# Kernel tuning notes

Hardware: AMD Instinct MI355X
Metric: run time of the kernel (lower is better)

The kernel has to match this reference:

```python
import jax, jax.numpy as jnp
import numpy as np

B, S, H = 1, 2048, 1024
NH, NKV, D = 8, 2, 128           # query heads, kv heads, head_dim
E, TOPK = 64, 6                   # experts per modality, top-k
IT, IV, IS = 512, 256, 1024       # text / vision expert inter, shared inter (=512*2)
THETA = 500000.0
SECTIONS = (22, 22, 20)           # h, w, t rotary freq split; sum = D//2
EPS = 1e-5


def rmsnorm(x, w):
    return x * w * jax.lax.rsqrt(jnp.mean(x * x, axis=-1, keepdims=True) + EPS)


def apply_mrope(x, positions):
    # x: [B,S,h,D]; positions: [3,B,S] (h, w, t position streams)
    inv_freq = 1.0 / (THETA ** (jnp.arange(0, D, 2, dtype=jnp.float32) / D))  # [D//2]
    axis_idx = np.repeat(np.arange(3), SECTIONS)              # which pos stream per freq band
    pos = jnp.transpose(positions[axis_idx], (1, 2, 0)).astype(jnp.float32)  # [B,S,D//2]
    freqs = pos * inv_freq
    cos = jnp.cos(freqs)[:, :, None, :]
    sin = jnp.sin(freqs)[:, :, None, :]
    x1, x2 = x[..., 0::2], x[..., 1::2]                       # interleaved (non-neox)
    o1 = x1 * cos - x2 * sin
    o2 = x1 * sin + x2 * cos
    return jnp.stack([o1, o2], axis=-1).reshape(x.shape)


def attention(x, positions, w_qkv, w_o):
    b, s, _ = x.shape
    qkv = x @ w_qkv
    q, k, v = jnp.split(qkv, [NH * D, NH * D + NKV * D], axis=-1)
    q = q.reshape(b, s, NH, D)
    k = k.reshape(b, s, NKV, D)
    v = v.reshape(b, s, NKV, D)
    q = apply_mrope(q, positions)
    k = apply_mrope(k, positions)
    rep = NH // NKV
    k = jnp.repeat(k, rep, axis=2)
    v = jnp.repeat(v, rep, axis=2)
    scores = jnp.einsum('bqhd,bkhd->bhqk', q, k) * (D ** -0.5)
    causal = jnp.tril(jnp.ones((s, s), bool))
    scores = jnp.where(causal, scores, -jnp.inf)
    attn = jax.nn.softmax(scores, axis=-1)
    out = jnp.einsum('bhqk,bkhd->bqhd', attn, v).reshape(b, s, NH * D)
    return out @ w_o


def mlp(x, wg, wu, wd):
    return (jax.nn.silu(x @ wg) * (x @ wu)) @ wd


def moe_branch(x, gate_w, bias, wg, wu, wd):
    # x: [T,H]; gate_w: [H,E] fp32; bias: [E] fp32 correction bias
    logits = x.astype(jnp.float32) @ gate_w                   # [T,E]
    scores = jax.nn.sigmoid(logits)
    _, topi = jax.lax.top_k(scores + bias[None, :], TOPK)     # bias only picks experts
    w = jnp.take_along_axis(scores, topi, axis=-1)            # weights from raw scores
    w = w / jnp.sum(w, axis=-1, keepdims=True)                # renormalize
    T = x.shape[0]
    gates = jnp.zeros((T, E), jnp.float32).at[jnp.arange(T)[:, None], topi].set(w)
    g = jax.nn.silu(jnp.einsum('th,ehi->eti', x, wg)) * jnp.einsum('th,ehi->eti', x, wu)
    g = g * gates.T[:, :, None].astype(x.dtype)               # fold routing weights pre-down-proj
    return jnp.einsum('eti,eih->th', g, wd)


def _forward(hidden_states, positions, visual_token_mask, w_qkv, w_o, ln1_w, ln2_w,
             text_gate_w, vision_gate_w, corr_bias, tw_gate, tw_up, tw_down,
             vw_gate, vw_up, vw_down, sw_gate, sw_up, sw_down):
    h = hidden_states + attention(rmsnorm(hidden_states, ln1_w), positions, w_qkv, w_o)
    x = rmsnorm(h, ln2_w).reshape(-1, H)                      # [T,H]
    shared = mlp(x, sw_gate, sw_up, sw_down)
    text_out = moe_branch(x, text_gate_w, corr_bias[0], tw_gate, tw_up, tw_down)
    vision_out = moe_branch(x, vision_gate_w, corr_bias[1], vw_gate, vw_up, vw_down)
    mask = visual_token_mask.reshape(-1, 1)
    moe_out = jnp.where(mask, vision_out, text_out) + shared
    return h + moe_out.reshape(h.shape)


def setup_inputs() -> dict:
    key = jax.random.key(0)
    ks = jax.random.split(key, 16)
    rn = lambda i, shape, s: jax.random.normal(ks[i], shape, jnp.float32) * s
    return dict(
        hidden_states=rn(0, (B, S, H), 1.0),
        positions=jnp.broadcast_to(jnp.arange(S, dtype=jnp.int32)[None, None, :], (3, B, S)),
        visual_token_mask=jax.random.bernoulli(ks[1], 0.3, (B, S)),
        w_qkv=rn(2, (H, (NH + 2 * NKV) * D), H ** -0.5),
        w_o=rn(3, (NH * D, H), (NH * D) ** -0.5),
        ln1_w=jnp.ones((H,), jnp.float32),
        ln2_w=jnp.ones((H,), jnp.float32),
        text_gate_w=rn(4, (H, E), H ** -0.5),
        vision_gate_w=rn(5, (H, E), H ** -0.5),
        corr_bias=rn(6, (2, E), 0.02),
        tw_gate=rn(7, (E, H, IT), H ** -0.5),
        tw_up=rn(8, (E, H, IT), H ** -0.5),
        tw_down=rn(9, (E, IT, H), IT ** -0.5),
        vw_gate=rn(10, (E, H, IV), H ** -0.5),
        vw_up=rn(11, (E, H, IV), H ** -0.5),
        vw_down=rn(12, (E, IV, H), IV ** -0.5),
        sw_gate=rn(13, (H, IS), H ** -0.5),
        sw_up=rn(14, (H, IS), H ** -0.5),
        sw_down=rn(15, (IS, H), IS ** -0.5),
    )


def reference(hidden_states, positions, visual_token_mask, w_qkv, w_o, ln1_w, ln2_w,
              text_gate_w, vision_gate_w, corr_bias, tw_gate, tw_up, tw_down,
              vw_gate, vw_up, vw_down, sw_gate, sw_up, sw_down):
    return _forward(hidden_states, positions, visual_token_mask, w_qkv, w_o, ln1_w, ln2_w,
                    text_gate_w, vision_gate_w, corr_bias, tw_gate, tw_up, tw_down,
                    vw_gate, vw_up, vw_down, sw_gate, sw_up, sw_down)
```

## Files before the change

kernel.cpp:

```cpp
#include <hip/hip_runtime.h>
#include <hip/hip_bf16.h>
#include <math.h>

#define TT   2048
#define HID  1024
#define NHEAD 8
#define NKVH  2
#define HD   128
#define QKVN 1536
#define NEXP 64
#define NTOP 6
#define I_T  512
#define I_V  256
#define I_S  1024
#define SBASE ((size_t)12288 * 512)
#define NCHUNK 576

typedef unsigned short u16;
typedef __attribute__((ext_vector_type(8))) short short8v;
typedef __attribute__((ext_vector_type(4))) float f32x4;

__device__ inline u16 f2bf(float f) {
  __hip_bfloat16 h = __float2bfloat16(f);
  return *reinterpret_cast<u16*>(&h);
}
__device__ inline float bfu2f(u16 u) {
  unsigned x = ((unsigned)u) << 16;
  return __uint_as_float(x);
}
__device__ inline void split2(float f, u16& h, u16& l) {
  h = f2bf(f);
  l = f2bf(f - bfu2f(h));
}
__device__ inline void split8(const float* f, u16* h, u16* l) {
#pragma unroll
  for (int i = 0; i < 8; ++i) split2(f[i], h[i], l[i]);
}

__device__ inline f32x4 mfma16(short8v a, short8v b, f32x4 c) {
  return __builtin_amdgcn_mfma_f32_16x16x32_bf16(a, b, c, 0, 0, 0);
}

__device__ inline void wload(const float* __restrict__ W, int ldw, int c0, int kc,
                             float4* r) {
  const int t = threadIdx.x;
  const int c4 = (t & 7) << 2;
  const int r0 = t >> 3;
#pragma unroll
  for (int j = 0; j < 4; ++j)
    r[j] = *(const float4*)&W[(size_t)(kc + r0 + j * 32) * ldw + c0 + c4];
}
__device__ inline void wwrite(const float4* r, u16* lds) {
  const int t = threadIdx.x;
  const int c4 = (t & 7) << 2;
  const int r0 = t >> 3;
#pragma unroll
  for (int j = 0; j < 4; ++j) {
    int k = r0 + j * 32;
    u16* dst = lds + ((k >> 3) * 32) * 8 + (k & 7);
    dst[(c4 + 0) * 8] = f2bf(r[j].x);
    dst[(c4 + 1) * 8] = f2bf(r[j].y);
    dst[(c4 + 2) * 8] = f2bf(r[j].z);
    dst[(c4 + 3) * 8] = f2bf(r[j].w);
  }
}

template<bool F32, bool BF, bool LO>
__global__ __launch_bounds__(256) void rmsnorm_kernel(const float* __restrict__ x,
                                                      const float* __restrict__ w,
                                                      float* __restrict__ o32,
                                                      u16* __restrict__ obfH,
                                                      u16* __restrict__ obfL) {
  const int row = blockIdx.x;
  const int t = threadIdx.x;
  const float4 v = *(const float4*)(x + (size_t)row * HID + t * 4);
  float ss = v.x*v.x + v.y*v.y + v.z*v.z + v.w*v.w;
#pragma unroll
  for (int m = 32; m >= 1; m >>= 1) ss += __shfl_xor(ss, m);
  __shared__ float red[4];
  __shared__ float rrs;
  if ((t & 63) == 0) red[t >> 6] = ss;
  __syncthreads();
  if (t == 0) rrs = rsqrtf((red[0] + red[1] + red[2] + red[3]) * (1.0f / HID) + 1e-5f);
  __syncthreads();
  const float rr = rrs;
  const float4 wv = *(const float4*)(w + t * 4);
  float o[4];
  o[0] = v.x * wv.x * rr; o[1] = v.y * wv.y * rr;
  o[2] = v.z * wv.z * rr; o[3] = v.w * wv.w * rr;
  if (F32) *(float4*)(o32 + (size_t)row * HID + t * 4) = *(float4*)o;
  if (BF) {
    u16 h[4], l[4];
#pragma unroll
    for (int i = 0; i < 4; ++i) split2(o[i], h[i], l[i]);
    *(uint2*)(obfH + (size_t)row * HID + t * 4) = *(uint2*)h;
    if (LO) *(uint2*)(obfL + (size_t)row * HID + t * 4) = *(uint2*)l;
  }
}

__global__ __launch_bounds__(256) void convert_w(const float* __restrict__ W, int N,
                                                 u16* __restrict__ PH,
                                                 u16* __restrict__ PL) {
  const int c = blockIdx.x * 256 + threadIdx.x;
  const int k8 = blockIdx.y;
  float f[8];
#pragma unroll
  for (int e = 0; e < 8; ++e) f[e] = W[(size_t)(k8 * 8 + e) * N + c];
  u16 h8[8], l8[8];
  split8(f, h8, l8);
  size_t gi = ((size_t)(c >> 5) * 128 + k8) * 256 + (size_t)(c & 31) * 8;
  *(uint4*)&PH[gi] = *(uint4*)h8;
  *(uint4*)&PL[gi] = *(uint4*)l8;
}

template<bool RES>
__global__ __launch_bounds__(256) void dense_split(const u16* __restrict__ AH,
                                                   const u16* __restrict__ AL,
                                                   const u16* __restrict__ WPH,
                                                   const u16* __restrict__ WPL,
                                                   const float* __restrict__ resid,
                                                   float* __restrict__ C, int N) {
  __shared__ u16 sWH[32768], sWL[32768];
  __shared__ u16 sAH[4096],  sAL[4096];
  const int t = threadIdx.x;
  const int cs = blockIdx.x;
  const int c0 = cs * 32;
  const int rows = TT / gridDim.y;
  const int mstart = blockIdx.y * rows, mend = mstart + rows;
  {
    const u16* gh = WPH + (size_t)cs * 32768;
    const u16* gl = WPL + (size_t)cs * 32768;
#pragma unroll
    for (int r = 0; r < 16; ++r) {
      int i8 = (t + 256 * r) * 8;
      *(uint4*)&sWH[i8] = *(const uint4*)&gh[i8];
      *(uint4*)&sWL[i8] = *(const uint4*)&gl[i8];
    }
  }
  const int w = t >> 6, lane = t & 63;
  const int rowHalf = (w & 1) << 4, colHalf = (w >> 1) << 4;
  for (int m0 = mstart; m0 < mend; m0 += 32) {
    f32x4 hh = {0.f,0.f,0.f,0.f}, hl = {0.f,0.f,0.f,0.f};
    f32x4 lh = {0.f,0.f,0.f,0.f}, ll = {0.f,0.f,0.f,0.f};
    for (int kc = 0; kc < HID; kc += 128) {
      __syncthreads();
#pragma unroll
      for (int r = 0; r < 2; ++r) {
        int task = t + 256 * r;
        int row = task >> 4, kg = task & 15;
        size_t g = (size_t)(m0 + row) * HID + kc + kg * 8;
        *(uint4*)&sAH[(kg * 32 + row) * 8] = *(const uint4*)&AH[g];
        *(uint4*)&sAL[(kg * 32 + row) * 8] = *(const uint4*)&AL[g];
      }
      __syncthreads();
#pragma unroll
      for (int ks = 0; ks < 4; ++ks) {
        int arow = rowHalf + (lane & 15);
        int akg = ks * 4 + (lane >> 4);
        short8v ah = *(const short8v*)&sAH[(akg * 32 + arow) * 8];
        short8v al = *(const short8v*)&sAL[(akg * 32 + arow) * 8];
        int wcol = colHalf + (lane & 15);
        int wkg = (kc >> 3) + ks * 4 + (lane >> 4);
        short8v bh = *(const short8v*)&sWH[(wkg * 32 + wcol) * 8];
        short8v bl = *(const short8v*)&sWL[(wkg * 32 + wcol) * 8];
        hh = mfma16(ah, bh, hh);
        hl = mfma16(ah, bl, hl);
        lh = mfma16(al, bh, lh);
        ll = mfma16(al, bl, ll);
      }
    }
    f32x4 acc = (hh + hl) + (lh + ll);
#pragma unroll
    for (int i = 0; i < 4; ++i) {
      int r = m0 + rowHalf + ((lane >> 4) << 2) + i;
      int c = c0 + colHalf + (lane & 15);
      float v = acc[i];
      if (RES) v += resid[(size_t)r * N + c];
      C[(size_t)r * N + c] = v;
    }
  }
}

__global__ __launch_bounds__(256) void pack_qkv(const float* __restrict__ qkv,
                                                const int* __restrict__ pos,
                                                u16* __restrict__ Qh, u16* __restrict__ Ql,
                                                u16* __restrict__ Kph, u16* __restrict__ Kpl,
                                                u16* __restrict__ Vph, u16* __restrict__ Vpl) {
  const int tile = blockIdx.x;
  const int t = threadIdx.x;
  __shared__ float cs[2048], sn[2048];
  for (int i = t; i < 2048; i += 256) {
    int tok32 = i >> 6, fi = i & 63;
    int tok = tile * 32 + tok32;
    int axis = (fi < 22) ? 0 : (fi < 44 ? 1 : 2);
    float posv = (float)pos[axis * TT + tok];
// ... 260 lines not shown
  float f[8];
#pragma unroll
  for (int j = 0; j < 8; ++j) f[j] = acc[j] * inv;
  split8(f, h8, l8);
  const size_t d = (size_t)(qb * 16 + row) * HID + head * HD + c8;
  *(uint4*)&aoH[d] = *(uint4*)h8;
  *(uint4*)&aoL[d] = *(uint4*)l8;
}

__global__ __launch_bounds__(256) void gate_kernel(const float* __restrict__ x2,
                                                   const int* __restrict__ vmask,
                                                   const float* __restrict__ tg,
                                                   const float* __restrict__ vg,
                                                   const float* __restrict__ cbias,
                                                   int* __restrict__ counts,
                                                   int* __restrict__ ptok,
                                                   float* __restrict__ pw) {
  const int tok = blockIdx.x;
  const int t = threadIdx.x;
  __shared__ float xs[HID];
  __shared__ float part[4][NEXP];
  __shared__ float sc[NEXP];
  __shared__ float sb[NEXP];
  *(float4*)&xs[t * 4] = *(const float4*)(x2 + (size_t)tok * HID + t * 4);
  __syncthreads();
  const int vis = (vmask[tok] != 0) ? 1 : 0;
  const float* gw = vis ? vg : tg;
  {
    const int e = t & 63, pr = t >> 6;
    float acc = 0.f;
    for (int h = pr * 256; h < (pr + 1) * 256; ++h) acc += xs[h] * gw[h * NEXP + e];
    part[pr][e] = acc;
  }
  __syncthreads();
  if (t < NEXP) {
    float a = part[0][t] + part[1][t] + part[2][t] + part[3][t];
    float s = 1.f / (1.f + expf(-a));
    sc[t] = s;
    sb[t] = s + cbias[vis * NEXP + t];
  }
  __syncthreads();
  if (t == 0) {
    int chosen[NTOP];
    unsigned long long usedm = 0ULL;
    float wsum = 0.f;
    for (int k = 0; k < NTOP; ++k) {
      float best = -1e30f; int bi = 0;
      for (int e = 0; e < NEXP; ++e) {
        if ((usedm >> e) & 1ULL) continue;
        if (sb[e] > best) { best = sb[e]; bi = e; }
      }
      usedm |= (1ULL << bi);
      chosen[k] = bi;
      wsum += sc[bi];
    }
    const float inv = 1.f / wsum;
    for (int k = 0; k < NTOP; ++k) {
      int e = chosen[k];
      int slot = vis * NEXP + e;
      int pos = atomicAdd(&counts[slot], 1);
      ptok[slot * TT + pos] = tok;
      pw[slot * TT + pos] = sc[e] * inv;
    }
  }
}

__global__ void scan_kernel(const int* __restrict__ counts, int* __restrict__ rowoff) {
  if (threadIdx.x == 0 && blockIdx.x == 0) {
    int s = 0;
    for (int i = 0; i < 128; ++i) { rowoff[i] = s; s += counts[i]; }
    rowoff[128] = s;
  }
}

template<int MODE>
__device__ inline void act_base(const int* rowoff, int slot, size_t& eb, int& stride) {
  if (MODE == 0) { eb = (size_t)rowoff[slot] * 512; stride = 512; }
  else if (MODE == 1) {
    int Rt = rowoff[64];
    eb = (size_t)Rt * 512 + (size_t)(rowoff[slot] - Rt) * 256; stride = 256;
  } else { eb = SBASE; stride = 1024; }
}

template<int IDIM, int MODE>
__global__ __launch_bounds__(256) void gateup_stream(const u16* __restrict__ X,
                                                     const float* __restrict__ WG,
                                                     const float* __restrict__ WU,
                                                     const int* __restrict__ counts,
                                                     const int* __restrict__ ptok,
                                                     const float* __restrict__ pw,
                                                     const int* __restrict__ rowoff,
                                                     u16* __restrict__ ACT) {
  __shared__ u16 sG[2][4096], sU[2][4096];
  __shared__ int toksL[256];
  __shared__ float twsL[256];
  const int c0 = blockIdx.x * 32;
  int cnt, mstart, mend, slot = 0;
  size_t eb; int stride;
  const float *wgp, *wup;
  if (MODE == 2) {
    cnt = TT; mstart = blockIdx.y * 256; mend = mstart + 256;
    eb = SBASE; stride = 1024;
    wgp = WG; wup = WU;
  } else {
    const int e = blockIdx.y;
    slot = (MODE == 1 ? NEXP : 0) + e;
    cnt = counts[slot];
    mstart = 0; mend = cnt;
    act_base<MODE>(rowoff, slot, eb, stride);
    wgp = WG + (size_t)e * HID * IDIM;
    wup = WU + (size_t)e * HID * IDIM;
  }
  if (mstart >= mend) return;
  const int w = threadIdx.x >> 6, lane = threadIdx.x & 63;
  const int lrow = lane & 15, loct = lane >> 4;

  for (int m0 = mstart; m0 < mend; m0 += 256) {
    {
      int gi = m0 + threadIdx.x;
      int tok = 0; float tw = 0.f;
      if (gi < cnt) {
        tok = (MODE == 2) ? gi : ptok[slot * TT + gi];
        tw  = (MODE == 2) ? 1.f : pw[slot * TT + gi];
      }
      toksL[threadIdx.x] = tok; twsL[threadIdx.x] = tw;
    }
    float4 rg[4], ru[4];
    wload(wgp, IDIM, c0, 0, rg);
    wload(wup, IDIM, c0, 0, ru);
    __syncthreads();
    wwrite(rg, sG[0]);
    wwrite(ru, sU[0]);
    const u16* xr[4];
#pragma unroll
    for (int tt = 0; tt < 4; ++tt)
      xr[tt] = X + (size_t)toksL[(w + tt * 4) * 16 + lrow] * HID;
    f32x4 aG[4][2], aU[4][2];
#pragma unroll
    for (int tt = 0; tt < 4; ++tt)
#pragma unroll
      for (int fr = 0; fr < 2; ++fr) {
        aG[tt][fr] = (f32x4){0.f,0.f,0.f,0.f};
        aU[tt][fr] = (f32x4){0.f,0.f,0.f,0.f};
      }
    __syncthreads();
    for (int c = 0; c < HID / 128; ++c) {
      const int cur = c & 1;
      if (c + 1 < HID / 128) {
        wload(wgp, IDIM, c0, (c + 1) * 128, rg);
        wload(wup, IDIM, c0, (c + 1) * 128, ru);
      }
#pragma unroll
      for (int ks = 0; ks < 4; ++ks) {
        const int boff = ((ks * 4 + loct) * 32 + lrow) * 8;
        short8v bg0 = *(const short8v*)&sG[cur][boff];
        short8v bg1 = *(const short8v*)&sG[cur][boff + 128];
        short8v bu0 = *(const short8v*)&sU[cur][boff];
        short8v bu1 = *(const short8v*)&sU[cur][boff + 128];
#pragma unroll
        for (int tt = 0; tt < 4; ++tt) {
          short8v a = *(const short8v*)&xr[tt][c * 128 + ks * 32 + loct * 8];
          aG[tt][0] = mfma16(a, bg0, aG[tt][0]);
          aG[tt][1] = mfma16(a, bg1, aG[tt][1]);
          aU[tt][0] = mfma16(a, bu0, aU[tt][0]);
          aU[tt][1] = mfma16(a, bu1, aU[tt][1]);
        }
      }
      if (c + 1 < HID / 128) {
        wwrite(rg, sG[cur ^ 1]);
        wwrite(ru, sU[cur ^ 1]);
      }
      __syncthreads();
    }
#pragma unroll
    for (int tt = 0; tt < 4; ++tt) {
      const int ti = w + tt * 4;
#pragma unroll
      for (int i = 0; i < 4; ++i) {
        const int r = loct * 4 + i;
        const int gi = m0 + ti * 16 + r;
        if (gi < cnt) {
          const float twv = twsL[ti * 16 + r];
#pragma unroll
          for (int fr = 0; fr < 2; ++fr) {
            float g = aG[tt][fr][i], u = aU[tt][fr][i];
            float a = g / (1.f + expf(-g)) * u * twv;
            ACT[eb + (size_t)gi * stride + c0 + fr * 16 + lrow] = f2bf(a);
          }
        }
      }
    }
    __syncthreads();
  }
}

template<int KDIM, int MODE>
__global__ __launch_bounds__(256) void down_stream(const u16* __restrict__ ACT,
                                                   const float* __restrict__ WD,
                                                   const int* __restrict__ counts,
                                                   const int* __restrict__ ptok,
                                                   const int* __restrict__ rowoff,
                                                   float* __restrict__ OUT) {
  __shared__ u16 sW[2][4096];
  __shared__ int toksL[256];
  const int c0 = blockIdx.x * 32;
  int cnt, mstart, mend, slot = 0;
  size_t eb; int stride;
  const float* wdp;
  if (MODE == 2) {
    cnt = TT; mstart = blockIdx.y * 256; mend = mstart + 256;
    eb = SBASE; stride = 1024;
    wdp = WD;
  } else {
    const int e = blockIdx.y;
    slot = (MODE == 1 ? NEXP : 0) + e;
    cnt = counts[slot];
    mstart = 0; mend = cnt;
    act_base<MODE>(rowoff, slot, eb, stride);
    wdp = WD + (size_t)e * KDIM * HID;
  }
  if (mstart >= mend) return;
  const int w = threadIdx.x >> 6, lane = threadIdx.x & 63;
  const int lrow = lane & 15, loct = lane >> 4;
  constexpr int NC = KDIM / 128;

  for (int m0 = mstart; m0 < mend; m0 += 256) {
    {
      int gi = m0 + threadIdx.x;
      int tok = 0;
      if (gi < cnt) tok = (MODE == 2) ? gi : ptok[slot * TT + gi];
      toksL[threadIdx.x] = tok;
    }
    float4 rw[4];
    wload(wdp, HID, c0, 0, rw);
    __syncthreads();
    wwrite(rw, sW[0]);
    const u16* ar[4];
#pragma unroll
    for (int tt = 0; tt < 4; ++tt) {
      int gi = m0 + (w + tt * 4) * 16 + lrow;
      int gc = (gi < cnt) ? gi : (cnt - 1);
      ar[tt] = ACT + eb + (size_t)gc * stride;
    }
    f32x4 acc[4][2];
#pragma unroll
    for (int tt = 0; tt < 4; ++tt)
#pragma unroll
      for (int fr = 0; fr < 2; ++fr) acc[tt][fr] = (f32x4){0.f,0.f,0.f,0.f};
    __syncthreads();
    for (int c = 0; c < NC; ++c) {
      const int cur = c & 1;
      if (c + 1 < NC) wload(wdp, HID, c0, (c + 1) * 128, rw);
#pragma unroll
      for (int ks = 0; ks < 4; ++ks) {
        const int boff = ((ks * 4 + loct) * 32 + lrow) * 8;
        short8v b0 = *(const short8v*)&sW[cur][boff];
        short8v b1 = *(const short8v*)&sW[cur][boff + 128];
#pragma unroll
        for (int tt = 0; tt < 4; ++tt) {
          short8v a = *(const short8v*)&ar[tt][c * 128 + ks * 32 + loct * 8];
          acc[tt][0] = mfma16(a, b0, acc[tt][0]);
          acc[tt][1] = mfma16(a, b1, acc[tt][1]);
        }
      }
      if (c + 1 < NC) wwrite(rw, sW[cur ^ 1]);
      __syncthreads();
    }
#pragma unroll
    for (int tt = 0; tt < 4; ++tt) {
      const int ti = w + tt * 4;
#pragma unroll
      for (int i = 0; i < 4; ++i) {
        const int r = loct * 4 + i;
        const int gi = m0 + ti * 16 + r;
        if (gi < cnt) {
          const int tok = toksL[ti * 16 + r];
#pragma unroll
          for (int fr = 0; fr < 2; ++fr)
            atomicAdd(&OUT[(size_t)tok * HID + c0 + fr * 16 + lrow], acc[tt][fr][i]);
        }
      }
    }
    __syncthreads();
  }
}

__global__ __launch_bounds__(256) void add2_kernel(const float* __restrict__ a,
                                                   const float* __restrict__ b,
                                                   float* __restrict__ out) {
  const size_t i = ((size_t)blockIdx.x * 256 + threadIdx.x) * 4;
  const float4 va = *(const float4*)(a + i);
  const float4 vb = *(const float4*)(b + i);
  float4 o;
  o.x = va.x + vb.x; o.y = va.y + vb.y; o.z = va.z + vb.z; o.w = va.w + vb.w;
  *(float4*)(out + i) = o;
}

extern "C" void kernel_launch(void* const* d_in, const int* in_sizes, int n_in,
                              void* d_out, int out_size, void* d_ws, size_t ws_size,
                              hipStream_t stream) {
  const float* hidden   = (const float*)d_in[0];
  const int*   positions= (const int*)d_in[1];
  const int*   vmask    = (const int*)d_in[2];
  const float* w_qkv    = (const float*)d_in[3];
  const float* w_o      = (const float*)d_in[4];
  const float* ln1      = (const float*)d_in[5];
  const float* ln2      = (const float*)d_in[6];
  const float* tgw      = (const float*)d_in[7];
  const float* vgw      = (const float*)d_in[8];
  const float* cbias    = (const float*)d_in[9];
  const float* twg      = (const float*)d_in[10];
  const float* twu      = (const float*)d_in[11];
  const float* twd      = (const float*)d_in[12];
  const float* vwg      = (const float*)d_in[13];
  const float* vwu      = (const float*)d_in[14];
  const float* vwd      = (const float*)d_in[15];
  const float* swg      = (const float*)d_in[16];
  const float* swu      = (const float*)d_in[17];
  const float* swd      = (const float*)d_in[18];
  float* out = (float*)d_out;

  char* ws = (char*)d_ws;
  size_t off = 0;
  auto alloc = [&](size_t bytes) -> void* {
    void* p = ws + off;
    off += (bytes + 255) & ~(size_t)255;
    return p;
  };
  u16*   xbh   = (u16*)alloc((size_t)TT * HID * 2);
  u16*   xbl   = (u16*)alloc((size_t)TT * HID * 2);
  float* qkv   = (float*)alloc((size_t)TT * QKVN * 4);
  u16*   aoH   = (u16*)alloc((size_t)TT * HID * 2);
  u16*   aoL   = (u16*)alloc((size_t)TT * HID * 2);
  float* hbuf  = (float*)alloc((size_t)TT * HID * 4);
  float* x2    = (float*)alloc((size_t)TT * HID * 4);
  u16*   xb2   = (u16*)alloc((size_t)TT * HID * 2);
  float* moe   = (float*)alloc((size_t)TT * HID * 4);
  u16*   ACT   = (u16*)alloc((SBASE + (size_t)TT * 1024) * 2);
  u16*   wqkvPH= (u16*)alloc((size_t)HID * QKVN * 2);
  u16*   wqkvPL= (u16*)alloc((size_t)HID * QKVN * 2);
  u16*   woPH  = (u16*)alloc((size_t)HID * HID * 2);
  u16*   woPL  = (u16*)alloc((size_t)HID * HID * 2);
  u16*   Qph   = (u16*)alloc((size_t)TT * HID * 2);
  u16*   Qpl   = (u16*)alloc((size_t)TT * HID * 2);
  u16*   Kph   = (u16*)alloc((size_t)NKVH * TT * HD * 2);
  u16*   Kpl   = (u16*)alloc((size_t)NKVH * TT * HD * 2);
  u16*   Vph   = (u16*)alloc((size_t)NKVH * TT * HD * 2);
  u16*   Vpl   = (u16*)alloc((size_t)NKVH * TT * HD * 2);
  float* Opart = (float*)alloc((size_t)NHEAD * NCHUNK * 16 * 128 * 4);
  float* Mpart = (float*)alloc((size_t)NHEAD * NCHUNK * 16 * 4);
  float* Lpart = (float*)alloc((size_t)NHEAD * NCHUNK * 16 * 4);
  int*   ctab  = (int*)alloc(NCHUNK * 4);
  int*   cstart= (int*)alloc((TT / 16) * 4);
  int*   counts= (int*)alloc(128 * 4);
  int*   rowoff= (int*)alloc(129 * 4);
  int*   ptok  = (int*)alloc((size_t)128 * TT * 4);
  float* pwgt  = (float*)alloc((size_t)128 * TT * 4);

  hipMemsetAsync(counts, 0, 128 * 4, stream);
  hipMemsetAsync(moe, 0, (size_t)TT * HID * 4, stream);

  chunk_setup<<<1, 64, 0, stream>>>(ctab, cstart);
  convert_w<<<dim3(QKVN / 256, 128), 256, 0, stream>>>(w_qkv, QKVN, wqkvPH, wqkvPL);
  convert_w<<<dim3(HID / 256, 128), 256, 0, stream>>>(w_o, HID, woPH, woPL);

  rmsnorm_kernel<false, true, true><<<TT, 256, 0, stream>>>(hidden, ln1, nullptr, xbh, xbl);
  dense_split<false><<<dim3(QKVN / 32, 8), 256, 0, stream>>>(xbh, xbl, wqkvPH, wqkvPL, nullptr, qkv, QKVN);
  pack_qkv<<<TT / 32, 256, 0, stream>>>(qkv, positions, Qph, Qpl, Kph, Kpl, Vph, Vpl);
  attn_part<<<dim3(NCHUNK, NKVH), 256, 0, stream>>>(Qph, Qpl, Kph, Kpl, Vph, Vpl, ctab, Opart, Mpart, Lpart);
  attn_combine<<<dim3(TT / 16, NHEAD), 256, 0, stream>>>(Opart, Mpart, Lpart, cstart, aoH, aoL);
  dense_split<true><<<dim3(HID / 32, 8), 256, 0, stream>>>(aoH, aoL, woPH, woPL, hidden, hbuf, HID);
  rmsnorm_kernel<true, true, false><<<TT, 256, 0, stream>>>(hbuf, ln2, x2, xb2, nullptr);
  gate_kernel<<<TT, 256, 0, stream>>>(x2, vmask, tgw, vgw, cbias, counts, ptok, pwgt);
  scan_kernel<<<1, 64, 0, stream>>>(counts, rowoff);

  gateup_stream<I_S, 2><<<dim3(I_S / 32, 8), 256, 0, stream>>>(xb2, swg, swu, nullptr, nullptr, nullptr, rowoff, ACT);
  gateup_stream<I_T, 0><<<dim3(I_T / 32, NEXP), 256, 0, stream>>>(xb2, twg, twu, counts, ptok, pwgt, rowoff, ACT);
  gateup_stream<I_V, 1><<<dim3(I_V / 32, NEXP), 256, 0, stream>>>(xb2, vwg, vwu, counts, ptok, pwgt, rowoff, ACT);

  down_stream<I_S, 2><<<dim3(HID / 32, 8), 256, 0, stream>>>(ACT, swd, nullptr, nullptr, rowoff, moe);
  down_stream<I_T, 0><<<dim3(HID / 32, NEXP), 256, 0, stream>>>(ACT, twd, counts, ptok, rowoff, moe);
  down_stream<I_V, 1><<<dim3(HID / 32, NEXP), 256, 0, stream>>>(ACT, vwd, counts, ptok, rowoff, moe);

  add2_kernel<<<(TT * HID) / 1024, 256, 0, stream>>>(hbuf, moe, out);
}
```

Baseline: 832.6 us.

## Merge MoE expert launches into single kernels and deepen weight prefetch

The three gate/up launches (shared, text, vision) are merged into one kernel, and likewise the three down launches, with each block choosing its branch from a flat block index. This removes launch gaps and lets light expert blocks overlap with heavy ones. The K loop is also unrolled by two, with two register sets of prefetched weights so loads run two chunks ahead. The extra prefetch registers may raise register pressure and lower occupancy.

```diff
diff --git a/kernel.cpp b/kernel.cpp
--- a/kernel.cpp
+++ b/kernel.cpp
@@ -537,34 +537,69 @@
   } else { eb = SBASE; stride = 1024; }
 }
 
+__device__ __forceinline__ void gu_mfma(const u16* sg, const u16* su,
+                                        const u16* const* xr, int c,
+                                        f32x4 (&aG)[4][2], f32x4 (&aU)[4][2],
+                                        int lrow, int loct) {
+#pragma unroll
+  for (int ks = 0; ks < 4; ++ks) {
+    const int boff = ((ks * 4 + loct) * 32 + lrow) * 8;
+    short8v bg0 = *(const short8v*)&sg[boff];
+    short8v bg1 = *(const short8v*)&sg[boff + 128];
+    short8v bu0 = *(const short8v*)&su[boff];
+    short8v bu1 = *(const short8v*)&su[boff + 128];
+#pragma unroll
+    for (int tt = 0; tt < 4; ++tt) {
+      short8v a = *(const short8v*)&xr[tt][c * 128 + ks * 32 + loct * 8];
+      aG[tt][0] = mfma16(a, bg0, aG[tt][0]);
+      aG[tt][1] = mfma16(a, bg1, aG[tt][1]);
+      aU[tt][0] = mfma16(a, bu0, aU[tt][0]);
+      aU[tt][1] = mfma16(a, bu1, aU[tt][1]);
+    }
+  }
+}
+
+__device__ __forceinline__ void d_mfma(const u16* sw, const u16* const* ar, int c,
+                                       f32x4 (&acc)[4][2], int lrow, int loct) {
+#pragma unroll
+  for (int ks = 0; ks < 4; ++ks) {
+    const int boff = ((ks * 4 + loct) * 32 + lrow) * 8;
+    short8v b0 = *(const short8v*)&sw[boff];
+    short8v b1 = *(const short8v*)&sw[boff + 128];
+#pragma unroll
+    for (int tt = 0; tt < 4; ++tt) {
+      short8v a = *(const short8v*)&ar[tt][c * 128 + ks * 32 + loct * 8];
+      acc[tt][0] = mfma16(a, b0, acc[tt][0]);
+      acc[tt][1] = mfma16(a, b1, acc[tt][1]);
+    }
+  }
+}
+
 template<int IDIM, int MODE>
-__global__ __launch_bounds__(256) void gateup_stream(const u16* __restrict__ X,
-                                                     const float* __restrict__ WG,
-                                                     const float* __restrict__ WU,
-                                                     const int* __restrict__ counts,
-                                                     const int* __restrict__ ptok,
-                                                     const float* __restrict__ pw,
-                                                     const int* __restrict__ rowoff,
-                                                     u16* __restrict__ ACT) {
-  __shared__ u16 sG[2][4096], sU[2][4096];
-  __shared__ int toksL[256];
-  __shared__ float twsL[256];
-  const int c0 = blockIdx.x * 32;
+__device__ __forceinline__ void gateup_body(int id, const u16* __restrict__ X,
+    const float* __restrict__ WG, const float* __restrict__ WU,
+    const int* __restrict__ counts, const int* __restrict__ ptok,
+    const float* __restrict__ pw, const int* __restrict__ rowoff,
+    u16* __restrict__ ACT,
+    u16 (&sG)[2][4096], u16 (&sU)[2][4096],
+    int (&toksL)[256], float (&twsL)[256]) {
+  constexpr int CH = IDIM / 32;
+  const int c0 = (id % CH) * 32;
+  const int eg = id / CH;
   int cnt, mstart, mend, slot = 0;
   size_t eb; int stride;
   const float *wgp, *wup;
   if (MODE == 2) {
-    cnt = TT; mstart = blockIdx.y * 256; mend = mstart + 256;
+    cnt = TT; mstart = eg * 256; mend = mstart + 256;
     eb = SBASE; stride = 1024;
     wgp = WG; wup = WU;
   } else {
-    const int e = blockIdx.y;
-    slot = (MODE == 1 ? NEXP : 0) + e;
+    slot = (MODE == 1 ? NEXP : 0) + eg;
     cnt = counts[slot];
     mstart = 0; mend = cnt;
     act_base<MODE>(rowoff, slot, eb, stride);
-    wgp = WG + (size_t)e * HID * IDIM;
-    wup = WU + (size_t)e * HID * IDIM;
+    wgp = WG + (size_t)eg * HID * IDIM;
+    wup = WU + (size_t)eg * HID * IDIM;
   }
   if (mstart >= mend) return;
   const int w = threadIdx.x >> 6, lane = threadIdx.x & 63;
@@ -580,12 +615,14 @@
       }
       toksL[threadIdx.x] = tok; twsL[threadIdx.x] = tw;
     }
-    float4 rg[4], ru[4];
-    wload(wgp, IDIM, c0, 0, rg);
-    wload(wup, IDIM, c0, 0, ru);
+    float4 rgA[4], ruA[4], rgB[4], ruB[4];
+    wload(wgp, IDIM, c0, 0, rgA);
+    wload(wup, IDIM, c0, 0, ruA);
     __syncthreads();
-    wwrite(rg, sG[0]);
-    wwrite(ru, sU[0]);
+    wload(wgp, IDIM, c0, 128, rgB);
+    wload(wup, IDIM, c0, 128, ruB);
+    wwrite(rgA, sG[0]);
+    wwrite(ruA, sU[0]);
     const u16* xr[4];
 #pragma unroll
     for (int tt = 0; tt < 4; ++tt)
@@ -599,32 +636,17 @@
         aU[tt][fr] = (f32x4){0.f,0.f,0.f,0.f};
       }
     __syncthreads();
-    for (int c = 0; c < HID / 128; ++c) {
-      const int cur = c & 1;
-      if (c + 1 < HID / 128) {
-        wload(wgp, IDIM, c0, (c + 1) * 128, rg);
-        wload(wup, IDIM, c0, (c + 1) * 128, ru);
-      }
-#pragma unroll
-      for (int ks = 0; ks < 4; ++ks) {
-        const int boff = ((ks * 4 + loct) * 32 + lrow) * 8;
-        short8v bg0 = *(const short8v*)&sG[cur][boff];
-        short8v bg1 = *(const short8v*)&sG[cur][boff + 128];
-        short8v bu0 = *(const short8v*)&sU[cur][boff];
-        short8v bu1 = *(const short8v*)&sU[cur][boff + 128];
-#pragma unroll
-        for (int tt = 0; tt < 4; ++tt) {
-          short8v a = *(const short8v*)&xr[tt][c * 128 + ks * 32 + loct * 8];
-          aG[tt][0] = mfma16(a, bg0, aG[tt][0]);
-          aG[tt][1] = mfma16(a, bg1, aG[tt][1]);
-          aU[tt][0] = mfma16(a, bu0, aU[tt][0]);
-          aU[tt][1] = mfma16(a, bu1, aU[tt][1]);
-        }
-      }
-      if (c + 1 < HID / 128) {
-        wwrite(rg, sG[cur ^ 1]);
-        wwrite(ru, sU[cur ^ 1]);
-      }
+#pragma unroll
+    for (int c = 0; c < 8; c += 2) {
+      if (c + 2 < 8) { wload(wgp, IDIM, c0, (c + 2) * 128, rgA);
+                       wload(wup, IDIM, c0, (c + 2) * 128, ruA); }
+      gu_mfma(sG[0], sU[0], xr, c, aG, aU, lrow, loct);
+      if (c + 1 < 8) { wwrite(rgB, sG[1]); wwrite(ruB, sU[1]); }
+      __syncthreads();
+      if (c + 3 < 8) { wload(wgp, IDIM, c0, (c + 3) * 128, rgB);
+                       wload(wup, IDIM, c0, (c + 3) * 128, ruB); }
+      if (c + 1 < 8) gu_mfma(sG[1], sU[1], xr, c + 1, aG, aU, lrow, loct);
+      if (c + 2 < 8) { wwrite(rgA, sG[0]); wwrite(ruA, sU[0]); }
       __syncthreads();
     }
 #pragma unroll
@@ -649,35 +671,52 @@
   }
 }
 
+__global__ __launch_bounds__(256) void gateup_fused(const u16* __restrict__ X,
+    const float* __restrict__ swg, const float* __restrict__ swu,
+    const float* __restrict__ twg, const float* __restrict__ twu,
+    const float* __restrict__ vwg, const float* __restrict__ vwu,
+    const int* __restrict__ counts, const int* __restrict__ ptok,
+    const float* __restrict__ pw, const int* __restrict__ rowoff,
+    u16* __restrict__ ACT) {
+  __shared__ u16 sG[2][4096], sU[2][4096];
+  __shared__ int toksL[256];
+  __shared__ float twsL[256];
+  const int b = blockIdx.x;
+  if (b < 1024)
+    gateup_body<I_T, 0>(b, X, twg, twu, counts, ptok, pw, rowoff, ACT, sG, sU, toksL, twsL);
+  else if (b < 1536)
+    gateup_body<I_V, 1>(b - 1024, X, vwg, vwu, counts, ptok, pw, rowoff, ACT, sG, sU, toksL, twsL);
+  else
+    gateup_body<I_S, 2>(b - 1536, X, swg, swu, counts, ptok, pw, rowoff, ACT, sG, sU, toksL, twsL);
+}
+
 template<int KDIM, int MODE>
-__global__ __launch_bounds__(256) void down_stream(const u16* __restrict__ ACT,
-                                                   const float* __restrict__ WD,
-                                                   const int* __restrict__ counts,
-                                                   const int* __restrict__ ptok,
-                                                   const int* __restrict__ rowoff,
-                                                   float* __restrict__ OUT) {
-  __shared__ u16 sW[2][4096];
-  __shared__ int toksL[256];
-  const int c0 = blockIdx.x * 32;
+__device__ __forceinline__ void down_body(int id, const u16* __restrict__ ACT,
+    const float* __restrict__ WD,
+    const int* __restrict__ counts, const int* __restrict__ ptok,
+    const int* __restrict__ rowoff, float* __restrict__ OUT,
+    u16 (&sW)[2][4096], int (&toksL)[256]) {
+  constexpr int CH = 32;
+  constexpr int NC = KDIM / 128;
+  const int c0 = (id % CH) * 32;
+  const int eg = id / CH;
   int cnt, mstart, mend, slot = 0;
   size_t eb; int stride;
   const float* wdp;
   if (MODE == 2) {
-    cnt = TT; mstart = blockIdx.y * 256; mend = mstart + 256;
+    cnt = TT; mstart = eg * 256; mend = mstart + 256;
     eb = SBASE; stride = 1024;
     wdp = WD;
   } else {
-    const int e = blockIdx.y;
-    slot = (MODE == 1 ? NEXP : 0) + e;
+    slot = (MODE == 1 ? NEXP : 0) + eg;
     cnt = counts[slot];
     mstart = 0; mend = cnt;
     act_base<MODE>(rowoff, slot, eb, stride);
-    wdp = WD + (size_t)e * KDIM * HID;
+    wdp = WD + (size_t)eg * KDIM * HID;
   }
   if (mstart >= mend) return;
   const int w = threadIdx.x >> 6, lane = threadIdx.x & 63;
   const int lrow = lane & 15, loct = lane >> 4;
-  constexpr int NC = KDIM / 128;
 
   for (int m0 = mstart; m0 < mend; m0 += 256) {
     {
@@ -686,10 +725,11 @@
       if (gi < cnt) tok = (MODE == 2) ? gi : ptok[slot * TT + gi];
       toksL[threadIdx.x] = tok;
     }
-    float4 rw[4];
-    wload(wdp, HID, c0, 0, rw);
+    float4 rwA[4], rwB[4];
+    wload(wdp, HID, c0, 0, rwA);
     __syncthreads();
-    wwrite(rw, sW[0]);
+    wload(wdp, HID, c0, 128, rwB);
+    wwrite(rwA, sW[0]);
     const u16* ar[4];
 #pragma unroll
     for (int tt = 0; tt < 4; ++tt) {
@@ -703,22 +743,15 @@
 #pragma unroll
       for (int fr = 0; fr < 2; ++fr) acc[tt][fr] = (f32x4){0.f,0.f,0.f,0.f};
     __syncthreads();
-    for (int c = 0; c < NC; ++c) {
-      const int cur = c & 1;
-      if (c + 1 < NC) wload(wdp, HID, c0, (c + 1) * 128, rw);
-#pragma unroll
-      for (int ks = 0; ks < 4; ++ks) {
-        const int boff = ((ks * 4 + loct) * 32 + lrow) * 8;
-        short8v b0 = *(const short8v*)&sW[cur][boff];
-        short8v b1 = *(const short8v*)&sW[cur][boff + 128];
-#pragma unroll
-        for (int tt = 0; tt < 4; ++tt) {
-          short8v a = *(const short8v*)&ar[tt][c * 128 + ks * 32 + loct * 8];
-          acc[tt][0] = mfma16(a, b0, acc[tt][0]);
-          acc[tt][1] = mfma16(a, b1, acc[tt][1]);
-        }
-      }
-      if (c + 1 < NC) wwrite(rw, sW[cur ^ 1]);
+#pragma unroll
+    for (int c = 0; c < NC; c += 2) {
+      if (c + 2 < NC) wload(wdp, HID, c0, (c + 2) * 128, rwA);
+      d_mfma(sW[0], ar, c, acc, lrow, loct);
+      if (c + 1 < NC) wwrite(rwB, sW[1]);
+      __syncthreads();
+      if (c + 3 < NC) wload(wdp, HID, c0, (c + 3) * 128, rwB);
+      if (c + 1 < NC) d_mfma(sW[1], ar, c + 1, acc, lrow, loct);
+      if (c + 2 < NC) wwrite(rwA, sW[0]);
       __syncthreads();
     }
 #pragma unroll
@@ -738,6 +771,22 @@
     }
     __syncthreads();
   }
+}
+
+__global__ __launch_bounds__(256) void down_fused(const u16* __restrict__ ACT,
+    const float* __restrict__ swd, const float* __restrict__ twd,
+    const float* __restrict__ vwd,
+    const int* __restrict__ counts, const int* __restrict__ ptok,
+    const int* __restrict__ rowoff, float* __restrict__ OUT) {
+  __shared__ u16 sW[2][4096];
+  __shared__ int toksL[256];
+  const int b = blockIdx.x;
+  if (b < 2048)
+    down_body<I_T, 0>(b, ACT, twd, counts, ptok, rowoff, OUT, sW, toksL);
+  else if (b < 4096)
+    down_body<I_V, 1>(b - 2048, ACT, vwd, counts, ptok, rowoff, OUT, sW, toksL);
+  else
+    down_body<I_S, 2>(b - 4096, ACT, swd, counts, ptok, rowoff, OUT, sW, toksL);
 }
 
 __global__ __launch_bounds__(256) void add2_kernel(const float* __restrict__ a,
@@ -829,13 +878,9 @@
   gate_kernel<<<TT, 256, 0, stream>>>(x2, vmask, tgw, vgw, cbias, counts, ptok, pwgt);
   scan_kernel<<<1, 64, 0, stream>>>(counts, rowoff);
 
-  gateup_stream<I_S, 2><<<dim3(I_S / 32, 8), 256, 0, stream>>>(xb2, swg, swu, nullptr, nullptr, nullptr, rowoff, ACT);
-  gateup_stream<I_T, 0><<<dim3(I_T / 32, NEXP), 256, 0, stream>>>(xb2, twg, twu, counts, ptok, pwgt, rowoff, ACT);
-  gateup_stream<I_V, 1><<<dim3(I_V / 32, NEXP), 256, 0, stream>>>(xb2, vwg, vwu, counts, ptok, pwgt, rowoff, ACT);
-
-  down_stream<I_S, 2><<<dim3(HID / 32, 8), 256, 0, stream>>>(ACT, swd, nullptr, nullptr, rowoff, moe);
-  down_stream<I_T, 0><<<dim3(HID / 32, NEXP), 256, 0, stream>>>(ACT, twd, counts, ptok, rowoff, moe);
-  down_stream<I_V, 1><<<dim3(HID / 32, NEXP), 256, 0, stream>>>(ACT, vwd, counts, ptok, rowoff, moe);
+  gateup_fused<<<1792, 256, 0, stream>>>(xb2, swg, swu, twg, twu, vwg, vwu,
+                                         counts, ptok, pwgt, rowoff, ACT);
+  down_fused<<<4352, 256, 0, stream>>>(ACT, swd, twd, vwd, counts, ptok, rowoff, moe);
 
   add2_kernel<<<(TT * HID) / 1024, 256, 0, stream>>>(hbuf, moe, out);
 }
```

Measured after the change: 848.4 us. Within noise of the previous version (+1.9%).

## Prepack MoE expert weights to bf16 tiles and double-buffer packed loads

Applied to the files above, without the earlier changes.

Adds a convert_w1 kernel that turns every text, vision and shared expert weight into bf16, laid out in the tiled order the MFMA loop consumes. The gate/up and down stream kernels then copy whole uint4 tiles straight into LDS with a two-stage unrolled software pipeline. This replaces the per-element fp32 load, bf16 convert and scattered 2-byte LDS stores. The trade-off is that the conversion runs on every call, so all expert weights are read in fp32, written in bf16 and read again, even for experts that receive no tokens.

```diff
diff --git a/kernel.cpp b/kernel.cpp
--- a/kernel.cpp
+++ b/kernel.cpp
@@ -39,30 +39,6 @@
 
 __device__ inline f32x4 mfma16(short8v a, short8v b, f32x4 c) {
   return __builtin_amdgcn_mfma_f32_16x16x32_bf16(a, b, c, 0, 0, 0);
-}
-
-__device__ inline void wload(const float* __restrict__ W, int ldw, int c0, int kc,
-                             float4* r) {
-  const int t = threadIdx.x;
-  const int c4 = (t & 7) << 2;
-  const int r0 = t >> 3;
-#pragma unroll
-  for (int j = 0; j < 4; ++j)
-    r[j] = *(const float4*)&W[(size_t)(kc + r0 + j * 32) * ldw + c0 + c4];
-}
-__device__ inline void wwrite(const float4* r, u16* lds) {
-  const int t = threadIdx.x;
-  const int c4 = (t & 7) << 2;
-  const int r0 = t >> 3;
-#pragma unroll
-  for (int j = 0; j < 4; ++j) {
-    int k = r0 + j * 32;
-    u16* dst = lds + ((k >> 3) * 32) * 8 + (k & 7);
-    dst[(c4 + 0) * 8] = f2bf(r[j].x);
-    dst[(c4 + 1) * 8] = f2bf(r[j].y);
-    dst[(c4 + 2) * 8] = f2bf(r[j].z);
-    dst[(c4 + 3) * 8] = f2bf(r[j].w);
-  }
 }
 
 template<bool F32, bool BF, bool LO>
@@ -111,6 +87,23 @@
   size_t gi = ((size_t)(c >> 5) * 128 + k8) * 256 + (size_t)(c & 31) * 8;
   *(uint4*)&PH[gi] = *(uint4*)h8;
   *(uint4*)&PL[gi] = *(uint4*)l8;
+}
+
+__global__ __launch_bounds__(256) void convert_w1(const float* __restrict__ W, int N,
+                                                  int K8, u16* __restrict__ P) {
+  const int c = blockIdx.x * 256 + threadIdx.x;
+  const int k8 = blockIdx.y;
+  const int e = blockIdx.z;
+  const float* Wp = W + (size_t)e * K8 * 8 * N;
+  u16* Pp = P + (size_t)e * K8 * 8 * N;
+  float f[8];
+#pragma unroll
+  for (int j = 0; j < 8; ++j) f[j] = Wp[(size_t)(k8 * 8 + j) * N + c];
+  u16 h8[8];
+#pragma unroll
+  for (int j = 0; j < 8; ++j) h8[j] = f2bf(f[j]);
+  size_t gi = ((size_t)(c >> 5) * K8 + k8) * 256 + (size_t)(c & 31) * 8;
+  *(uint4*)&Pp[gi] = *(uint4*)h8;
 }
 
 template<bool RES>
@@ -537,10 +530,69 @@
   } else { eb = SBASE; stride = 1024; }
 }
 
+__device__ __forceinline__ void wloadp(const u16* __restrict__ Pb, int c, uint4* r) {
+  const uint4* s = (const uint4*)(Pb + (size_t)c * 4096);
+  r[0] = s[threadIdx.x];
+  r[1] = s[threadIdx.x + 256];
+}
+__device__ __forceinline__ void wwritep(const uint4* r, u16* lds) {
+  uint4* d = (uint4*)lds;
+  d[threadIdx.x] = r[0];
+  d[threadIdx.x + 256] = r[1];
+}
+
+__device__ __forceinline__ void gu_mfma2(const u16* sg, const u16* su,
+                                         const u16* const* xr, int c,
+                                         f32x4 (&aG)[4][2], f32x4 (&aU)[4][2],
+                                         int lrow, int loct) {
+  short8v a[4][4];
+#pragma unroll
+  for (int ks = 0; ks < 4; ++ks)
+#pragma unroll
+    for (int tt = 0; tt < 4; ++tt)
+      a[ks][tt] = *(const short8v*)&xr[tt][c * 128 + ks * 32 + loct * 8];
+#pragma unroll
+  for (int ks = 0; ks < 4; ++ks) {
+    const int boff = ((ks * 4 + loct) * 32 + lrow) * 8;
+    short8v bg0 = *(const short8v*)&sg[boff];
+    short8v bg1 = *(const short8v*)&sg[boff + 128];
+    short8v bu0 = *(const short8v*)&su[boff];
+    short8v bu1 = *(const short8v*)&su[boff + 128];
+#pragma unroll
+    for (int tt = 0; tt < 4; ++tt) {
+      aG[tt][0] = mfma16(a[ks][tt], bg0, aG[tt][0]);
+      aG[tt][1] = mfma16(a[ks][tt], bg1, aG[tt][1]);
+      aU[tt][0] = mfma16(a[ks][tt], bu0, aU[tt][0]);
+      aU[tt][1] = mfma16(a[ks][tt], bu1, aU[tt][1]);
+    }
+  }
+}
+
+__device__ __forceinline__ void d_mfma2(const u16* sw, const u16* const* ar, int c,
+                                        f32x4 (&acc)[4][2], int lrow, int loct) {
+  short8v a[4][4];
+#pragma unroll
+  for (int ks = 0; ks < 4; ++ks)
+#pragma unroll
+    for (int tt = 0; tt < 4; ++tt)
+      a[ks][tt] = *(const short8v*)&ar[tt][c * 128 + ks * 32 + loct * 8];
+#pragma unroll
+  for (int ks = 0; ks < 4; ++ks) {
+    const int boff = ((ks * 4 + loct) * 32 + lrow) * 8;
+    short8v b0 = *(const short8v*)&sw[boff];
+    short8v b1 = *(const short8v*)&sw[boff + 128];
+#pragma unroll
+    for (int tt = 0; tt < 4; ++tt) {
+      acc[tt][0] = mfma16(a[ks][tt], b0, acc[tt][0]);
+      acc[tt][1] = mfma16(a[ks][tt], b1, acc[tt][1]);
+    }
+  }
+}
+
 template<int IDIM, int MODE>
 __global__ __launch_bounds__(256) void gateup_stream(const u16* __restrict__ X,
-                                                     const float* __restrict__ WG,
-                                                     const float* __restrict__ WU,
+                                                     const u16* __restrict__ PG,
+                                                     const u16* __restrict__ PU,
                                                      const int* __restrict__ counts,
                                                      const int* __restrict__ ptok,
                                                      const float* __restrict__ pw,
@@ -549,22 +601,24 @@
   __shared__ u16 sG[2][4096], sU[2][4096];
   __shared__ int toksL[256];
   __shared__ float twsL[256];
-  const int c0 = blockIdx.x * 32;
+  const int cch = blockIdx.x;
+  const int c0 = cch * 32;
   int cnt, mstart, mend, slot = 0;
   size_t eb; int stride;
-  const float *wgp, *wup;
+  const u16 *pg, *pu;
   if (MODE == 2) {
     cnt = TT; mstart = blockIdx.y * 256; mend = mstart + 256;
     eb = SBASE; stride = 1024;
-    wgp = WG; wup = WU;
+    pg = PG + (size_t)cch * HID * 32;
+    pu = PU + (size_t)cch * HID * 32;
   } else {
     const int e = blockIdx.y;
     slot = (MODE == 1 ? NEXP : 0) + e;
     cnt = counts[slot];
     mstart = 0; mend = cnt;
     act_base<MODE>(rowoff, slot, eb, stride);
-    wgp = WG + (size_t)e * HID * IDIM;
-    wup = WU + (size_t)e * HID * IDIM;
+    pg = PG + (size_t)e * HID * IDIM + (size_t)cch * HID * 32;
+    pu = PU + (size_t)e * HID * IDIM + (size_t)cch * HID * 32;
   }
   if (mstart >= mend) return;
   const int w = threadIdx.x >> 6, lane = threadIdx.x & 63;
@@ -580,12 +634,11 @@
       }
       toksL[threadIdx.x] = tok; twsL[threadIdx.x] = tw;
     }
-    float4 rg[4], ru[4];
-    wload(wgp, IDIM, c0, 0, rg);
-    wload(wup, IDIM, c0, 0, ru);
+    uint4 rgA[2], ruA[2], rgB[2], ruB[2];
+    wloadp(pg, 0, rgA); wloadp(pu, 0, ruA);
     __syncthreads();
-    wwrite(rg, sG[0]);
-    wwrite(ru, sU[0]);
+    wloadp(pg, 1, rgB); wloadp(pu, 1, ruB);
+    wwritep(rgA, sG[0]); wwritep(ruA, sU[0]);
     const u16* xr[4];
 #pragma unroll
     for (int tt = 0; tt < 4; ++tt)
@@ -599,32 +652,15 @@
         aU[tt][fr] = (f32x4){0.f,0.f,0.f,0.f};
       }
     __syncthreads();
-    for (int c = 0; c < HID / 128; ++c) {
-      const int cur = c & 1;
-      if (c + 1 < HID / 128) {
-        wload(wgp, IDIM, c0, (c + 1) * 128, rg);
-        wload(wup, IDIM, c0, (c + 1) * 128, ru);
-      }
-#pragma unroll
-      for (int ks = 0; ks < 4; ++ks) {
-        const int boff = ((ks * 4 + loct) * 32 + lrow) * 8;
-        short8v bg0 = *(const short8v*)&sG[cur][boff];
-        short8v bg1 = *(const short8v*)&sG[cur][boff + 128];
-        short8v bu0 = *(const short8v*)&sU[cur][boff];
-        short8v bu1 = *(const short8v*)&sU[cur][boff + 128];
-#pragma unroll
-        for (int tt = 0; tt < 4; ++tt) {
-          short8v a = *(const short8v*)&xr[tt][c * 128 + ks * 32 + loct * 8];
-          aG[tt][0] = mfma16(a, bg0, aG[tt][0]);
-          aG[tt][1] = mfma16(a, bg1, aG[tt][1]);
-          aU[tt][0] = mfma16(a, bu0, aU[tt][0]);
-          aU[tt][1] = mfma16(a, bu1, aU[tt][1]);
-        }
-      }
-      if (c + 1 < HID / 128) {
-        wwrite(rg, sG[cur ^ 1]);
-        wwrite(ru, sU[cur ^ 1]);
-      }
+#pragma unroll
+    for (int c = 0; c < 8; c += 2) {
+      if (c + 2 < 8) { wloadp(pg, c + 2, rgA); wloadp(pu, c + 2, ruA); }
+      gu_mfma2(sG[0], sU[0], xr, c, aG, aU, lrow, loct);
+      if (c + 1 < 8) { wwritep(rgB, sG[1]); wwritep(ruB, sU[1]); }
+      __syncthreads();
+      if (c + 3 < 8) { wloadp(pg, c + 3, rgB); wloadp(pu, c + 3, ruB); }
+      if (c + 1 < 8) gu_mfma2(sG[1], sU[1], xr, c + 1, aG, aU, lrow, loct);
+      if (c + 2 < 8) { wwritep(rgA, sG[0]); wwritep(ruA, sU[0]); }
       __syncthreads();
     }
 #pragma unroll
@@ -651,33 +687,34 @@
 
 template<int KDIM, int MODE>
 __global__ __launch_bounds__(256) void down_stream(const u16* __restrict__ ACT,
-                                                   const float* __restrict__ WD,
+                                                   const u16* __restrict__ PD,
                                                    const int* __restrict__ counts,
                                                    const int* __restrict__ ptok,
                                                    const int* __restrict__ rowoff,
                                                    float* __restrict__ OUT) {
   __shared__ u16 sW[2][4096];
   __shared__ int toksL[256];
-  const int c0 = blockIdx.x * 32;
+  constexpr int NC = KDIM / 128;
+  const int cch = blockIdx.x;
+  const int c0 = cch * 32;
   int cnt, mstart, mend, slot = 0;
   size_t eb; int stride;
-  const float* wdp;
+  const u16* pd;
   if (MODE == 2) {
     cnt = TT; mstart = blockIdx.y * 256; mend = mstart + 256;
     eb = SBASE; stride = 1024;
-    wdp = WD;
+    pd = PD + (size_t)cch * KDIM * 32;
   } else {
     const int e = blockIdx.y;
     slot = (MODE == 1 ? NEXP : 0) + e;
     cnt = counts[slot];
     mstart = 0; mend = cnt;
     act_base<MODE>(rowoff, slot, eb, stride);
-    wdp = WD + (size_t)e * KDIM * HID;
+    pd = PD + (size_t)e * KDIM * HID + (size_t)cch * KDIM * 32;
   }
   if (mstart >= mend) return;
   const int w = threadIdx.x >> 6, lane = threadIdx.x & 63;
   const int lrow = lane & 15, loct = lane >> 4;
-  constexpr int NC = KDIM / 128;
 
   for (int m0 = mstart; m0 < mend; m0 += 256) {
     {
@@ -686,10 +723,11 @@
       if (gi < cnt) tok = (MODE == 2) ? gi : ptok[slot * TT + gi];
       toksL[threadIdx.x] = tok;
     }
-    float4 rw[4];
-    wload(wdp, HID, c0, 0, rw);
+    uint4 rwA[2], rwB[2];
+    wloadp(pd, 0, rwA);
     __syncthreads();
-    wwrite(rw, sW[0]);
+    if (NC > 1) wloadp(pd, 1, rwB);
+    wwritep(rwA, sW[0]);
     const u16* ar[4];
 #pragma unroll
     for (int tt = 0; tt < 4; ++tt) {
@@ -703,22 +741,15 @@
 #pragma unroll
       for (int fr = 0; fr < 2; ++fr) acc[tt][fr] = (f32x4){0.f,0.f,0.f,0.f};
     __syncthreads();
-    for (int c = 0; c < NC; ++c) {
-      const int cur = c & 1;
-      if (c + 1 < NC) wload(wdp, HID, c0, (c + 1) * 128, rw);
-#pragma unroll
-      for (int ks = 0; ks < 4; ++ks) {
-        const int boff = ((ks * 4 + loct) * 32 + lrow) * 8;
-        short8v b0 = *(const short8v*)&sW[cur][boff];
-        short8v b1 = *(const short8v*)&sW[cur][boff + 128];
-#pragma unroll
-        for (int tt = 0; tt < 4; ++tt) {
-          short8v a = *(const short8v*)&ar[tt][c * 128 + ks * 32 + loct * 8];
-          acc[tt][0] = mfma16(a, b0, acc[tt][0]);
-          acc[tt][1] = mfma16(a, b1, acc[tt][1]);
-        }
-      }
-      if (c + 1 < NC) wwrite(rw, sW[cur ^ 1]);
+#pragma unroll
+    for (int c = 0; c < NC; c += 2) {
+      if (c + 2 < NC) wloadp(pd, c + 2, rwA);
+      d_mfma2(sW[0], ar, c, acc, lrow, loct);
+      if (c + 1 < NC) wwritep(rwB, sW[1]);
+      __syncthreads();
+      if (c + 3 < NC) wloadp(pd, c + 3, rwB);
+      if (c + 1 < NC) d_mfma2(sW[1], ar, c + 1, acc, lrow, loct);
+      if (c + 2 < NC) wwritep(rwA, sW[0]);
       __syncthreads();
     }
 #pragma unroll
@@ -811,6 +842,15 @@
   int*   rowoff= (int*)alloc(129 * 4);
   int*   ptok  = (int*)alloc((size_t)128 * TT * 4);
   float* pwgt  = (float*)alloc((size_t)128 * TT * 4);
+  u16*   twgP  = (u16*)alloc((size_t)NEXP * HID * I_T * 2);
+  u16*   twuP  = (u16*)alloc((size_t)NEXP * HID * I_T * 2);
+  u16*   vwgP  = (u16*)alloc((size_t)NEXP * HID * I_V * 2);
+  u16*   vwuP  = (u16*)alloc((size_t)NEXP * HID * I_V * 2);
+  u16*   swgP  = (u16*)alloc((size_t)HID * I_S * 2);
+  u16*   swuP  = (u16*)alloc((size_t)HID * I_S * 2);
+  u16*   twdP  = (u16*)alloc((size_t)NEXP * I_T * HID * 2);
+  u16*   vwdP  = (u16*)alloc((size_t)NEXP * I_V * HID * 2);
+  u16*   swdP  = (u16*)alloc((size_t)I_S * HID * 2);
 
   hipMemsetAsync(counts, 0, 128 * 4, stream);
   hipMemsetAsync(moe, 0, (size_t)TT * HID * 4, stream);
@@ -818,6 +858,15 @@
   chunk_setup<<<1, 64, 0, stream>>>(ctab, cstart);
   convert_w<<<dim3(QKVN / 256, 128), 256, 0, stream>>>(w_qkv, QKVN, wqkvPH, wqkvPL);
   convert_w<<<dim3(HID / 256, 128), 256, 0, stream>>>(w_o, HID, woPH, woPL);
+  convert_w1<<<dim3(I_T / 256, HID / 8, NEXP), 256, 0, stream>>>(twg, I_T, HID / 8, twgP);
+  convert_w1<<<dim3(I_T / 256, HID / 8, NEXP), 256, 0, stream>>>(twu, I_T, HID / 8, twuP);
+  convert_w1<<<dim3(I_V / 256, HID / 8, NEXP), 256, 0, stream>>>(vwg, I_V, HID / 8, vwgP);
+  convert_w1<<<dim3(I_V / 256, HID / 8, NEXP), 256, 0, stream>>>(vwu, I_V, HID / 8, vwuP);
+  convert_w1<<<dim3(I_S / 256, HID / 8, 1), 256, 0, stream>>>(swg, I_S, HID / 8, swgP);
+  convert_w1<<<dim3(I_S / 256, HID / 8, 1), 256, 0, stream>>>(swu, I_S, HID / 8, swuP);
+  convert_w1<<<dim3(HID / 256, I_T / 8, NEXP), 256, 0, stream>>>(twd, HID, I_T / 8, twdP);
+  convert_w1<<<dim3(HID / 256, I_V / 8, NEXP), 256, 0, stream>>>(vwd, HID, I_V / 8, vwdP);
+  convert_w1<<<dim3(HID / 256, I_S / 8, 1), 256, 0, stream>>>(swd, HID, I_S / 8, swdP);
 
   rmsnorm_kernel<false, true, true><<<TT, 256, 0, stream>>>(hidden, ln1, nullptr, xbh, xbl);
   dense_split<false><<<dim3(QKVN / 32, 8), 256, 0, stream>>>(xbh, xbl, wqkvPH, wqkvPL, nullptr, qkv, QKVN);
@@ -829,13 +878,13 @@
   gate_kernel<<<TT, 256, 0, stream>>>(x2, vmask, tgw, vgw, cbias, counts, ptok, pwgt);
   scan_kernel<<<1, 64, 0, stream>>>(counts, rowoff);
 
-  gateup_stream<I_S, 2><<<dim3(I_S / 32, 8), 256, 0, stream>>>(xb2, swg, swu, nullptr, nullptr, nullptr, rowoff, ACT);
-  gateup_stream<I_T, 0><<<dim3(I_T / 32, NEXP), 256, 0, stream>>>(xb2, twg, twu, counts, ptok, pwgt, rowoff, ACT);
-  gateup_stream<I_V, 1><<<dim3(I_V / 32, NEXP), 256, 0, stream>>>(xb2, vwg, vwu, counts, ptok, pwgt, rowoff, ACT);
-
-  down_stream<I_S, 2><<<dim3(HID / 32, 8), 256, 0, stream>>>(ACT, swd, nullptr, nullptr, rowoff, moe);
-  down_stream<I_T, 0><<<dim3(HID / 32, NEXP), 256, 0, stream>>>(ACT, twd, counts, ptok, rowoff, moe);
-  down_stream<I_V, 1><<<dim3(HID / 32, NEXP), 256, 0, stream>>>(ACT, vwd, counts, ptok, rowoff, moe);
+  gateup_stream<I_S, 2><<<dim3(I_S / 32, 8), 256, 0, stream>>>(xb2, swgP, swuP, nullptr, nullptr, nullptr, rowoff, ACT);
+  gateup_stream<I_T, 0><<<dim3(I_T / 32, NEXP), 256, 0, stream>>>(xb2, twgP, twuP, counts, ptok, pwgt, rowoff, ACT);
+  gateup_stream<I_V, 1><<<dim3(I_V / 32, NEXP), 256, 0, stream>>>(xb2, vwgP, vwuP, counts, ptok, pwgt, rowoff, ACT);
+
+  down_stream<I_S, 2><<<dim3(HID / 32, 8), 256, 0, stream>>>(ACT, swdP, nullptr, nullptr, rowoff, moe);
+  down_stream<I_T, 0><<<dim3(HID / 32, NEXP), 256, 0, stream>>>(ACT, twdP, counts, ptok, rowoff, moe);
+  down_stream<I_V, 1><<<dim3(HID / 32, NEXP), 256, 0, stream>>>(ACT, vwdP, counts, ptok, rowoff, moe);
 
   add2_kernel<<<(TT * HID) / 1024, 256, 0, stream>>>(hbuf, moe, out);
 }
```

Result: slower. 985.2 us (+18.3%).
